# Performance work log

Measured on AMD Instinct MI355X. Metric: run time of the kernel, lower is better.

Reference implementation:

```python
import jax, jax.numpy as jnp
import numpy as np

H = 32  # hidden size


def _lstm_layer(x_sbi, w_ih, w_hh, b_ih, b_hh):
    # x_sbi: [S, B, in]; w_ih: [4H, in]; w_hh: [4H, H] (torch gate order i,f,g,o)
    S, B, _ = x_sbi.shape
    # precompute input projections for all timesteps: [S, B, 4H]
    xg = jnp.einsum('sbi,gi->sbg', x_sbi, w_ih) + (b_ih + b_hh)

    def step(carry, xg_t):
        h, c = carry
        gates = xg_t + h @ w_hh.T  # [B, 4H]
        i, f, g, o = jnp.split(gates, 4, axis=-1)
        i = jax.nn.sigmoid(i)
        f = jax.nn.sigmoid(f)
        g = jnp.tanh(g)
        o = jax.nn.sigmoid(o)
        c = f * c + i * g
        h = o * jnp.tanh(c)
        return (h, c), h

    h0 = jnp.zeros((B, H), x_sbi.dtype)
    c0 = jnp.zeros((B, H), x_sbi.dtype)
    (h_last, _), hs = jax.lax.scan(step, (h0, c0), xg)
    return hs, h_last  # hs: [S, B, H]


def setup_inputs() -> dict:
    key = jax.random.key(0)
    ks = jax.random.split(key, 12)
    B, S = 4096, 512
    s = 1.0 / np.sqrt(H)  # torch default uniform(-1/sqrt(H), 1/sqrt(H))
    u = lambda k, shape: jax.random.uniform(k, shape, jnp.float32, -s, s)
    return {
        'x': jax.random.normal(ks[0], (B, S, 1), jnp.float32),
        'w_ih0': u(ks[1], (4 * H, 1)),
        'w_hh0': u(ks[2], (4 * H, H)),
        'b_ih0': u(ks[3], (4 * H,)),
        'b_hh0': u(ks[4], (4 * H,)),
        'w_ih1': u(ks[5], (4 * H, H)),
        'w_hh1': u(ks[6], (4 * H, H)),
        'b_ih1': u(ks[7], (4 * H,)),
        'b_hh1': u(ks[8], (4 * H,)),
        'fc1_w': u(ks[9], (16, H)),
        'fc1_b': u(ks[9], (16,)),
        'fc2_w': u(ks[10], (1, 16)),
        'fc2_b': u(ks[11], (1,)),
    }


def reference(x, w_ih0, w_hh0, b_ih0, b_hh0, w_ih1, w_hh1, b_ih1, b_hh1,
              fc1_w, fc1_b, fc2_w, fc2_b):
    x_sbi = jnp.swapaxes(x, 0, 1)  # [S, B, 1]
    hs1, _ = _lstm_layer(x_sbi, w_ih0, w_hh0, b_ih0, b_hh0)
    _, h_last = _lstm_layer(hs1, w_ih1, w_hh1, b_ih1, b_hh1)  # last timestep of layer 2
    y = h_last @ fc1_w.T + fc1_b
    y = jnp.where(y >= 0, y, 0.2 * y)  # leaky_relu(0.2)
    y = y @ fc2_w.T + fc2_b
    return y  # [B, 1]
```

## Files before the change

kernel.cpp:

```cpp
#include <hip/hip_runtime.h>

#define H 32
#define SEQ 512
#define BM 16
#define NTHREADS 512
#define HSTRIDE 40

typedef _Float16 half8 __attribute__((ext_vector_type(8)));
typedef __attribute__((ext_vector_type(4))) float f32x4;

#define L2E 1.44269504088896340736f

__device__ __forceinline__ float rcp_(float x)  { return __builtin_amdgcn_rcpf(x); }
__device__ __forceinline__ float exp2_(float x) { return __builtin_amdgcn_exp2f(x); }

__global__ __launch_bounds__(NTHREADS, 2) void lstm_kernel(
    const float* __restrict__ x,
    const float* __restrict__ w_ih0,
    const float* __restrict__ w_hh0,
    const float* __restrict__ b_ih0, const float* __restrict__ b_hh0,
    const float* __restrict__ w_ih1,
    const float* __restrict__ w_hh1,
    const float* __restrict__ b_ih1, const float* __restrict__ b_hh1,
    const float* __restrict__ fc1_w,
    const float* __restrict__ fc1_b,
    const float* __restrict__ fc2_w,
    const float* __restrict__ fc2_b,
    float* __restrict__ out)
{
    __shared__ __align__(16) float    xbufT[SEQ * BM];
    __shared__ __align__(16) _Float16 h1s[2][BM * HSTRIDE];
    __shared__ __align__(16) _Float16 h2s[2][BM * HSTRIDE];
    __shared__ __align__(16) float    h2f[BM * 33];
    __shared__ __align__(16) float    yb[BM * 17];

    const int tid  = threadIdx.x;
    const int lane = tid & 63;
    const int wv   = tid >> 6;
    const int c    = lane & 15;
    const int q    = lane >> 4;
    const int r0   = blockIdx.x * BM;

    {
        const int row = tid >> 5;
        const int s0  = (tid & 31) * 16;
        const float* xr = x + (size_t)(r0 + row) * SEQ + s0;
        #pragma unroll
        for (int i = 0; i < 16; i += 4) {
            float4 v = *(const float4*)&xr[i];
            xbufT[(s0 + i + 0) * BM + row] = v.x;
            xbufT[(s0 + i + 1) * BM + row] = v.y;
            xbufT[(s0 + i + 2) * BM + row] = v.z;
            xbufT[(s0 + i + 3) * BM + row] = v.w;
        }
    }
    for (int i = tid; i < BM * HSTRIDE; i += NTHREADS) {
        h1s[0][i] = (_Float16)0.f; h1s[1][i] = (_Float16)0.f;
        h2s[0][i] = (_Float16)0.f; h2s[1][i] = (_Float16)0.f;
    }

    const float gsc[4] = { -L2E, -L2E, 2.f * L2E, -L2E };
    const int worig = (c & 3) * H + 4 * wv + (c >> 2);
    const float wsc = gsc[c & 3];
    const int kb = 8 * q;
    half8 w0h, w0l, wih, wil, whh, whl;
    {
        const float* p = &w_hh0[worig * H + kb];
        #pragma unroll
        for (int j = 0; j < 8; ++j) { float v = p[j] * wsc; _Float16 h = (_Float16)v; w0h[j] = h; w0l[j] = (_Float16)(v - (float)h); }
        p = &w_ih1[worig * H + kb];
        #pragma unroll
        for (int j = 0; j < 8; ++j) { float v = p[j] * wsc; _Float16 h = (_Float16)v; wih[j] = h; wil[j] = (_Float16)(v - (float)h); }
        p = &w_hh1[worig * H + kb];
        #pragma unroll
        for (int j = 0; j < 8; ++j) { float v = p[j] * wsc; _Float16 h = (_Float16)v; whh[j] = h; whl[j] = (_Float16)(v - (float)h); }
    }

    const int m = c;
    const int u = 4 * wv + q;
    f32x4 bias1v, bias2v;
    float wx[4];
    #pragma unroll
    for (int g = 0; g < 4; ++g) {
        bias1v[g] = (b_ih0[g * H + u] + b_hh0[g * H + u]) * gsc[g];
        bias2v[g] = (b_ih1[g * H + u] + b_hh1[g * H + u]) * gsc[g];
        wx[g]     = w_ih0[g * H + u] * gsc[g];
    }
    float c1 = 0.f, c2 = 0.f, h2last = 0.f;

    const int fofs = c * HSTRIDE + kb;
    const int hofs = m * HSTRIDE + u;

    __syncthreads();

    auto cell = [&](const f32x4& g, float& cst) -> float {
        float ei = exp2_(g[0]);
        float ef = exp2_(g[1]);
        float eg = exp2_(g[2]);
        float eo = exp2_(g[3]);
        float A  = 1.f + ei;
        float F  = 1.f + ef;
        float Gp = eg + 1.f, Gm = eg - 1.f;
        float t1 = A * Gp;
        float num = fmaf(cst, t1, Gm * F);
        float cn  = num * rcp_(F * t1);
        cn = fminf(fmaxf(cn, -12.f), 12.f);
        cst = cn;
        float ec = exp2_(cn * (2.f * L2E));
        return (ec - 1.f) * rcp_((1.f + eo) * (ec + 1.f));
    };

    auto do_step = [&](const _Float16* __restrict__ h1r, const _Float16* __restrict__ h2r,
                       _Float16* __restrict__ h1w, _Float16* __restrict__ h2w,
                       int t, bool ew1, bool ew2) {
        half8 a1 = *(const half8*)(h1r + fofs);
        half8 a2 = *(const half8*)(h2r + fofs);
        float xv = 0.f;
        if (ew1) xv = xbufT[t * BM + m];
        f32x4 g1 = bias1v, g2a = bias2v;
        f32x4 g2b = {0.f, 0.f, 0.f, 0.f};
        g1  = __builtin_amdgcn_mfma_f32_16x16x32_f16(w0h, a1, g1,  0, 0, 0);
        g2a = __builtin_amdgcn_mfma_f32_16x16x32_f16(wih, a1, g2a, 0, 0, 0);
        g2b = __builtin_amdgcn_mfma_f32_16x16x32_f16(whh, a2, g2b, 0, 0, 0);
        g1  = __builtin_amdgcn_mfma_f32_16x16x32_f16(w0l, a1, g1,  0, 0, 0);
        g2a = __builtin_amdgcn_mfma_f32_16x16x32_f16(wil, a1, g2a, 0, 0, 0);
        g2b = __builtin_amdgcn_mfma_f32_16x16x32_f16(whl, a2, g2b, 0, 0, 0);
        if (ew1) {
            #pragma unroll
            for (int j = 0; j < 4; ++j) g1[j] = fmaf(xv, wx[j], g1[j]);
            float h1v = cell(g1, c1);
            h1w[hofs] = (_Float16)h1v;
        }
        if (ew2) {
            f32x4 g2;
            #pragma unroll
            for (int j = 0; j < 4; ++j) g2[j] = g2a[j] + g2b[j];
            float h2v = cell(g2, c2);
            h2last = h2v;
            h2w[hofs] = (_Float16)h2v;
        }
        __syncthreads();
    };

    do_step(h1s[0], h2s[0], h1s[1], h2s[1], 0, true, false);
    for (int tt = 0; tt < 255; ++tt) {
        int t = 1 + 2 * tt;
        do_step(h1s[1], h2s[1], h1s[0], h2s[0], t,     true, true);
        do_step(h1s[0], h2s[0], h1s[1], h2s[1], t + 1, true, true);
    }
    do_step(h1s[1], h2s[1], h1s[0], h2s[0], 511, true, true);
    do_step(h1s[0], h2s[0], h1s[1], h2s[1], 512, false, true);

    h2f[m * 33 + u] = h2last;
    __syncthreads();
    if (tid < BM * 16) {
        int rr = tid >> 4, j = tid & 15;
        float acc = fc1_b[j];
        #pragma unroll
        for (int k = 0; k < H; ++k) acc += fc1_w[j * H + k] * h2f[rr * 33 + k];
        acc = acc >= 0.f ? acc : 0.2f * acc;
        yb[rr * 17 + j] = acc * fc2_w[j];
    }
    __syncthreads();
    if (tid < BM) {
        float acc = fc2_b[0];
        #pragma unroll
        for (int j = 0; j < 16; ++j) acc += yb[tid * 17 + j];
        out[r0 + tid] = acc;
    }
}

extern "C" void kernel_launch(void* const* d_in, const int* in_sizes, int n_in,
                              void* d_out, int out_size, void* d_ws, size_t ws_size,
                              hipStream_t stream) {
    const float* x     = (const float*)d_in[0];
    const float* w_ih0 = (const float*)d_in[1];
    const float* w_hh0 = (const float*)d_in[2];
    const float* b_ih0 = (const float*)d_in[3];
    const float* b_hh0 = (const float*)d_in[4];
    const float* w_ih1 = (const float*)d_in[5];
    const float* w_hh1 = (const float*)d_in[6];
    const float* b_ih1 = (const float*)d_in[7];
    const float* b_hh1 = (const float*)d_in[8];
    const float* fc1_w = (const float*)d_in[9];
    const float* fc1_b = (const float*)d_in[10];
    const float* fc2_w = (const float*)d_in[11];
    const float* fc2_b = (const float*)d_in[12];
    float* out = (float*)d_out;

    const int B = in_sizes[0] / SEQ;
    hipLaunchKernelGGL(lstm_kernel, dim3(B / BM), dim3(NTHREADS), 0, stream,
                       x, w_ih0, w_hh0, b_ih0, b_hh0, w_ih1, w_hh1, b_ih1, b_hh1,
                       fc1_w, fc1_b, fc2_w, fc2_b, out);
}
```

Before: 272.6 us.

## Split LSTM layers across two wave groups with 1024-thread blocks

Doubles the block to 16 waves and gives layer 1 and layer 2 separate wave groups. Each wave now holds weights for only one layer and runs a single cell update per step, where before it ran both. This shortens the per-step critical path and frees registers, at the cost of a larger barrier across 16 waves and possibly fewer resident blocks per CU. The clamp is also changed to a med3 instruction.

```diff
diff --git a/kernel.cpp b/kernel.cpp
--- a/kernel.cpp
+++ b/kernel.cpp
@@ -3,7 +3,7 @@
 #define H 32
 #define SEQ 512
 #define BM 16
-#define NTHREADS 512
+#define NTHREADS 1024
 #define HSTRIDE 40
 
 typedef _Float16 half8 __attribute__((ext_vector_type(8)));
@@ -14,7 +14,7 @@
 __device__ __forceinline__ float rcp_(float x)  { return __builtin_amdgcn_rcpf(x); }
 __device__ __forceinline__ float exp2_(float x) { return __builtin_amdgcn_exp2f(x); }
 
-__global__ __launch_bounds__(NTHREADS, 2) void lstm_kernel(
+__global__ __launch_bounds__(NTHREADS, 4) void lstm_kernel(
     const float* __restrict__ x,
     const float* __restrict__ w_ih0,
     const float* __restrict__ w_hh0,
@@ -37,16 +37,18 @@
     const int tid  = threadIdx.x;
     const int lane = tid & 63;
     const int wv   = tid >> 6;
+    const int grp  = wv >> 3;
+    const int tw   = wv & 7;
     const int c    = lane & 15;
     const int q    = lane >> 4;
     const int r0   = blockIdx.x * BM;
 
     {
-        const int row = tid >> 5;
-        const int s0  = (tid & 31) * 16;
+        const int row = tid >> 6;
+        const int s0  = (tid & 63) * 8;
         const float* xr = x + (size_t)(r0 + row) * SEQ + s0;
         #pragma unroll
-        for (int i = 0; i < 16; i += 4) {
+        for (int i = 0; i < 8; i += 4) {
             float4 v = *(const float4*)&xr[i];
             xbufT[(s0 + i + 0) * BM + row] = v.x;
             xbufT[(s0 + i + 1) * BM + row] = v.y;
@@ -60,40 +62,44 @@
     }
 
     const float gsc[4] = { -L2E, -L2E, 2.f * L2E, -L2E };
-    const int worig = (c & 3) * H + 4 * wv + (c >> 2);
+    const int worig = (c & 3) * H + 4 * tw + (c >> 2);
     const float wsc = gsc[c & 3];
     const int kb = 8 * q;
-    half8 w0h, w0l, wih, wil, whh, whl;
-    {
+    const int m = c;
+    const int u = 4 * tw + q;
+
+    half8 fA, fB, fC, fD;
+    f32x4 biasv;
+    float wx[4] = {0.f, 0.f, 0.f, 0.f};
+    if (grp == 0) {
         const float* p = &w_hh0[worig * H + kb];
         #pragma unroll
-        for (int j = 0; j < 8; ++j) { float v = p[j] * wsc; _Float16 h = (_Float16)v; w0h[j] = h; w0l[j] = (_Float16)(v - (float)h); }
-        p = &w_ih1[worig * H + kb];
-        #pragma unroll
-        for (int j = 0; j < 8; ++j) { float v = p[j] * wsc; _Float16 h = (_Float16)v; wih[j] = h; wil[j] = (_Float16)(v - (float)h); }
+        for (int j = 0; j < 8; ++j) { float v = p[j] * wsc; _Float16 h = (_Float16)v; fA[j] = h; fB[j] = (_Float16)(v - (float)h); }
+        #pragma unroll
+        for (int g = 0; g < 4; ++g) {
+            biasv[g] = (b_ih0[g * H + u] + b_hh0[g * H + u]) * gsc[g];
+            wx[g]    = w_ih0[g * H + u] * gsc[g];
+        }
+    } else {
+        const float* p = &w_ih1[worig * H + kb];
+        #pragma unroll
+        for (int j = 0; j < 8; ++j) { float v = p[j] * wsc; _Float16 h = (_Float16)v; fA[j] = h; fB[j] = (_Float16)(v - (float)h); }
         p = &w_hh1[worig * H + kb];
         #pragma unroll
-        for (int j = 0; j < 8; ++j) { float v = p[j] * wsc; _Float16 h = (_Float16)v; whh[j] = h; whl[j] = (_Float16)(v - (float)h); }
-    }
-
-    const int m = c;
-    const int u = 4 * wv + q;
-    f32x4 bias1v, bias2v;
-    float wx[4];
-    #pragma unroll
-    for (int g = 0; g < 4; ++g) {
-        bias1v[g] = (b_ih0[g * H + u] + b_hh0[g * H + u]) * gsc[g];
-        bias2v[g] = (b_ih1[g * H + u] + b_hh1[g * H + u]) * gsc[g];
-        wx[g]     = w_ih0[g * H + u] * gsc[g];
-    }
-    float c1 = 0.f, c2 = 0.f, h2last = 0.f;
+        for (int j = 0; j < 8; ++j) { float v = p[j] * wsc; _Float16 h = (_Float16)v; fC[j] = h; fD[j] = (_Float16)(v - (float)h); }
+        #pragma unroll
+        for (int g = 0; g < 4; ++g)
+            biasv[g] = (b_ih1[g * H + u] + b_hh1[g * H + u]) * gsc[g];
+    }
+
+    float cst = 0.f, h2last = 0.f;
 
     const int fofs = c * HSTRIDE + kb;
     const int hofs = m * HSTRIDE + u;
 
     __syncthreads();
 
-    auto cell = [&](const f32x4& g, float& cst) -> float {
+    auto cell = [&](const f32x4& g) -> float {
         float ei = exp2_(g[0]);
         float ef = exp2_(g[1]);
         float eg = exp2_(g[2]);
@@ -104,7 +110,7 @@
         float t1 = A * Gp;
         float num = fmaf(cst, t1, Gm * F);
         float cn  = num * rcp_(F * t1);
-        cn = fminf(fmaxf(cn, -12.f), 12.f);
+        cn = __builtin_amdgcn_fmed3f(cn, -12.f, 12.f);
         cst = cn;
         float ec = exp2_(cn * (2.f * L2E));
         return (ec - 1.f) * rcp_((1.f + eo) * (ec + 1.f));
@@ -112,32 +118,36 @@
 
     auto do_step = [&](const _Float16* __restrict__ h1r, const _Float16* __restrict__ h2r,
                        _Float16* __restrict__ h1w, _Float16* __restrict__ h2w,
-                       int t, bool ew1, bool ew2) {
-        half8 a1 = *(const half8*)(h1r + fofs);
-        half8 a2 = *(const half8*)(h2r + fofs);
-        float xv = 0.f;
-        if (ew1) xv = xbufT[t * BM + m];
-        f32x4 g1 = bias1v, g2a = bias2v;
-        f32x4 g2b = {0.f, 0.f, 0.f, 0.f};
-        g1  = __builtin_amdgcn_mfma_f32_16x16x32_f16(w0h, a1, g1,  0, 0, 0);
-        g2a = __builtin_amdgcn_mfma_f32_16x16x32_f16(wih, a1, g2a, 0, 0, 0);
-        g2b = __builtin_amdgcn_mfma_f32_16x16x32_f16(whh, a2, g2b, 0, 0, 0);
-        g1  = __builtin_amdgcn_mfma_f32_16x16x32_f16(w0l, a1, g1,  0, 0, 0);
-        g2a = __builtin_amdgcn_mfma_f32_16x16x32_f16(wil, a1, g2a, 0, 0, 0);
-        g2b = __builtin_amdgcn_mfma_f32_16x16x32_f16(whl, a2, g2b, 0, 0, 0);
-        if (ew1) {
-            #pragma unroll
-            for (int j = 0; j < 4; ++j) g1[j] = fmaf(xv, wx[j], g1[j]);
-            float h1v = cell(g1, c1);
-            h1w[hofs] = (_Float16)h1v;
-        }
-        if (ew2) {
-            f32x4 g2;
-            #pragma unroll
-            for (int j = 0; j < 4; ++j) g2[j] = g2a[j] + g2b[j];
-            float h2v = cell(g2, c2);
-            h2last = h2v;
-            h2w[hofs] = (_Float16)h2v;
+                       int t, bool e1, bool e2) {
+        if (grp == 0) {
+            if (e1) {
+                half8 a1 = *(const half8*)(h1r + fofs);
+                float xv = xbufT[t * BM + m];
+                f32x4 g1 = biasv;
+                g1 = __builtin_amdgcn_mfma_f32_16x16x32_f16(fA, a1, g1, 0, 0, 0);
+                g1 = __builtin_amdgcn_mfma_f32_16x16x32_f16(fB, a1, g1, 0, 0, 0);
+                #pragma unroll
+                for (int j = 0; j < 4; ++j) g1[j] = fmaf(xv, wx[j], g1[j]);
+                float h1v = cell(g1);
+                h1w[hofs] = (_Float16)h1v;
+            }
+        } else {
+            if (e2) {
+                half8 a1 = *(const half8*)(h1r + fofs);
+                half8 a2 = *(const half8*)(h2r + fofs);
+                f32x4 ga = biasv;
+                f32x4 gb = {0.f, 0.f, 0.f, 0.f};
+                ga = __builtin_amdgcn_mfma_f32_16x16x32_f16(fA, a1, ga, 0, 0, 0);
+                gb = __builtin_amdgcn_mfma_f32_16x16x32_f16(fC, a2, gb, 0, 0, 0);
+                ga = __builtin_amdgcn_mfma_f32_16x16x32_f16(fB, a1, ga, 0, 0, 0);
+                gb = __builtin_amdgcn_mfma_f32_16x16x32_f16(fD, a2, gb, 0, 0, 0);
+                f32x4 g2;
+                #pragma unroll
+                for (int j = 0; j < 4; ++j) g2[j] = ga[j] + gb[j];
+                float h2v = cell(g2);
+                h2last = h2v;
+                h2w[hofs] = (_Float16)h2v;
+            }
         }
         __syncthreads();
     };
@@ -151,7 +161,7 @@
     do_step(h1s[1], h2s[1], h1s[0], h2s[0], 511, true, true);
     do_step(h1s[0], h2s[0], h1s[1], h2s[1], 512, false, true);
 
-    h2f[m * 33 + u] = h2last;
+    if (grp == 1) h2f[m * 33 + u] = h2last;
     __syncthreads();
     if (tid < BM * 16) {
         int rr = tid >> 4, j = tid & 15;
```

Result: slower. 291.7 us (+7.0%).

## Halve rows per block and rebalance gate tiles across lanes via bpermute

Applied to the files above, without the earlier changes.

Each block now handles 8 batch rows with 4 waves instead of 16 rows with 8 waves, so the grid doubles. Each wave issues two sets of MFMA gate tiles (A and B hidden-unit halves) whose valid columns are merged with ds_bpermute, so every lane still does exactly one LSTM cell. The intent is a cheaper per-step barrier across fewer waves, and letting two independent blocks interleave on a CU to hide recurrence latency. The cost is twice the MFMA count per wave, with half the MFMA columns wasted on zero rows, plus the cross-lane permute. The clamp is also switched to a med3 instruction.

```diff
diff --git a/kernel.cpp b/kernel.cpp
--- a/kernel.cpp
+++ b/kernel.cpp
@@ -2,8 +2,8 @@
 
 #define H 32
 #define SEQ 512
-#define BM 16
-#define NTHREADS 512
+#define NR 8
+#define NTHREADS 256
 #define HSTRIDE 40
 
 typedef _Float16 half8 __attribute__((ext_vector_type(8)));
@@ -13,6 +13,10 @@
 
 __device__ __forceinline__ float rcp_(float x)  { return __builtin_amdgcn_rcpf(x); }
 __device__ __forceinline__ float exp2_(float x) { return __builtin_amdgcn_exp2f(x); }
+__device__ __forceinline__ float bperm_f(int idx, float v) {
+    return __int_as_float(__builtin_amdgcn_ds_bpermute(idx, __float_as_int(v)));
+}
+#define MFMA16(A, B, C) __builtin_amdgcn_mfma_f32_16x16x32_f16((A), (B), (C), 0, 0, 0)
 
 __global__ __launch_bounds__(NTHREADS, 2) void lstm_kernel(
     const float* __restrict__ x,
@@ -28,18 +32,18 @@
     const float* __restrict__ fc2_b,
     float* __restrict__ out)
 {
-    __shared__ __align__(16) float    xbufT[SEQ * BM];
-    __shared__ __align__(16) _Float16 h1s[2][BM * HSTRIDE];
-    __shared__ __align__(16) _Float16 h2s[2][BM * HSTRIDE];
-    __shared__ __align__(16) float    h2f[BM * 33];
-    __shared__ __align__(16) float    yb[BM * 17];
+    __shared__ __align__(16) float    xbufT[SEQ * NR];
+    __shared__ __align__(16) _Float16 h1s[2][16 * HSTRIDE];
+    __shared__ __align__(16) _Float16 h2s[2][16 * HSTRIDE];
+    __shared__ __align__(16) float    h2f[NR * 33];
+    __shared__ __align__(16) float    yb[NR * 17];
 
     const int tid  = threadIdx.x;
     const int lane = tid & 63;
     const int wv   = tid >> 6;
     const int c    = lane & 15;
     const int q    = lane >> 4;
-    const int r0   = blockIdx.x * BM;
+    const int r0   = blockIdx.x * NR;
 
     {
         const int row = tid >> 5;
@@ -48,48 +52,71 @@
         #pragma unroll
         for (int i = 0; i < 16; i += 4) {
             float4 v = *(const float4*)&xr[i];
-            xbufT[(s0 + i + 0) * BM + row] = v.x;
-            xbufT[(s0 + i + 1) * BM + row] = v.y;
-            xbufT[(s0 + i + 2) * BM + row] = v.z;
-            xbufT[(s0 + i + 3) * BM + row] = v.w;
-        }
-    }
-    for (int i = tid; i < BM * HSTRIDE; i += NTHREADS) {
+            xbufT[(s0 + i + 0) * NR + row] = v.x;
+            xbufT[(s0 + i + 1) * NR + row] = v.y;
+            xbufT[(s0 + i + 2) * NR + row] = v.z;
+            xbufT[(s0 + i + 3) * NR + row] = v.w;
+        }
+    }
+    for (int i = tid; i < 16 * HSTRIDE; i += NTHREADS) {
         h1s[0][i] = (_Float16)0.f; h1s[1][i] = (_Float16)0.f;
         h2s[0][i] = (_Float16)0.f; h2s[1][i] = (_Float16)0.f;
     }
 
     const float gsc[4] = { -L2E, -L2E, 2.f * L2E, -L2E };
-    const int worig = (c & 3) * H + 4 * wv + (c >> 2);
+    const int kb  = 8 * q;
     const float wsc = gsc[c & 3];
-    const int kb = 8 * q;
-    half8 w0h, w0l, wih, wil, whh, whl;
+
+    half8 w0hA, w0lA, w0hB, w0lB;
+    half8 wihA, wilA, wihB, wilB;
+    half8 whhA, whlA, whhB, whlB;
     {
-        const float* p = &w_hh0[worig * H + kb];
-        #pragma unroll
-        for (int j = 0; j < 8; ++j) { float v = p[j] * wsc; _Float16 h = (_Float16)v; w0h[j] = h; w0l[j] = (_Float16)(v - (float)h); }
-        p = &w_ih1[worig * H + kb];
-        #pragma unroll
-        for (int j = 0; j < 8; ++j) { float v = p[j] * wsc; _Float16 h = (_Float16)v; wih[j] = h; wil[j] = (_Float16)(v - (float)h); }
-        p = &w_hh1[worig * H + kb];
-        #pragma unroll
-        for (int j = 0; j < 8; ++j) { float v = p[j] * wsc; _Float16 h = (_Float16)v; whh[j] = h; whl[j] = (_Float16)(v - (float)h); }
-    }
-
-    const int m = c;
-    const int u = 4 * wv + q;
-    f32x4 bias1v, bias2v;
+        const int wrA = (c & 3) * H + 4 * wv + (c >> 2);
+        const int wrB = (c & 3) * H + 4 * (wv + 4) + (c >> 2);
+        const float *pA, *pB;
+        pA = &w_hh0[wrA * H + kb]; pB = &w_hh0[wrB * H + kb];
+        #pragma unroll
+        for (int j = 0; j < 8; ++j) {
+            float vA = pA[j] * wsc; _Float16 hA = (_Float16)vA; w0hA[j] = hA; w0lA[j] = (_Float16)(vA - (float)hA);
+            float vB = pB[j] * wsc; _Float16 hB = (_Float16)vB; w0hB[j] = hB; w0lB[j] = (_Float16)(vB - (float)hB);
+        }
+        pA = &w_ih1[wrA * H + kb]; pB = &w_ih1[wrB * H + kb];
+        #pragma unroll
+        for (int j = 0; j < 8; ++j) {
+            float vA = pA[j] * wsc; _Float16 hA = (_Float16)vA; wihA[j] = hA; wilA[j] = (_Float16)(vA - (float)hA);
+            float vB = pB[j] * wsc; _Float16 hB = (_Float16)vB; wihB[j] = hB; wilB[j] = (_Float16)(vB - (float)hB);
+        }
+        pA = &w_hh1[wrA * H + kb]; pB = &w_hh1[wrB * H + kb];
+        #pragma unroll
+        for (int j = 0; j < 8; ++j) {
+            float vA = pA[j] * wsc; _Float16 hA = (_Float16)vA; whhA[j] = hA; whlA[j] = (_Float16)(vA - (float)hA);
+            float vB = pB[j] * wsc; _Float16 hB = (_Float16)vB; whhB[j] = hB; whlB[j] = (_Float16)(vB - (float)hB);
+        }
+    }
+
+    f32x4 b1A, b1B, b2A, b2B;
+    {
+        const int uA = 4 * wv + q, uB = 4 * (wv + 4) + q;
+        #pragma unroll
+        for (int j = 0; j < 4; ++j) {
+            b1A[j] = (b_ih0[j * H + uA] + b_hh0[j * H + uA]) * gsc[j];
+            b1B[j] = (b_ih0[j * H + uB] + b_hh0[j * H + uB]) * gsc[j];
+            b2A[j] = (b_ih1[j * H + uA] + b_hh1[j * H + uA]) * gsc[j];
+            b2B[j] = (b_ih1[j * H + uB] + b_hh1[j * H + uB]) * gsc[j];
+        }
+    }
+
+    const int prow  = lane & 7;
+    const int upost = 4 * (wv + 4 * ((lane >> 3) & 1)) + (lane >> 4);
     float wx[4];
     #pragma unroll
-    for (int g = 0; g < 4; ++g) {
-        bias1v[g] = (b_ih0[g * H + u] + b_hh0[g * H + u]) * gsc[g];
-        bias2v[g] = (b_ih1[g * H + u] + b_hh1[g * H + u]) * gsc[g];
-        wx[g]     = w_ih0[g * H + u] * gsc[g];
-    }
+    for (int j = 0; j < 4; ++j) wx[j] = w_ih0[j * H + upost] * gsc[j];
+
     float c1 = 0.f, c2 = 0.f, h2last = 0.f;
 
-    const int fofs = c * HSTRIDE + kb;
-    const int hofs = m * HSTRIDE + u;
+    const int fofs  = c * HSTRIDE + kb;
+    const int whofs = prow * HSTRIDE + upost;
+    const int bpi   = (lane & ~8) * 4;
 
     __syncthreads();
 
@@ -104,40 +131,52 @@
         float t1 = A * Gp;
         float num = fmaf(cst, t1, Gm * F);
         float cn  = num * rcp_(F * t1);
-        cn = fminf(fmaxf(cn, -12.f), 12.f);
+        cn = __builtin_amdgcn_fmed3f(cn, -12.f, 12.f);
         cst = cn;
         float ec = exp2_(cn * (2.f * L2E));
         return (ec - 1.f) * rcp_((1.f + eo) * (ec + 1.f));
     };
 
+    const bool takeB = (lane & 8) != 0;
+    auto rebal = [&](const f32x4& A, const f32x4& B) -> f32x4 {
+        f32x4 r;
+        #pragma unroll
+        for (int j = 0; j < 4; ++j) {
+            float pb = bperm_f(bpi, B[j]);
+            r[j] = takeB ? pb : A[j];
+        }
+        return r;
+    };
+
     auto do_step = [&](const _Float16* __restrict__ h1r, const _Float16* __restrict__ h2r,
                        _Float16* __restrict__ h1w, _Float16* __restrict__ h2w,
-                       int t, bool ew1, bool ew2) {
+                       int t, bool e1, bool e2) {
         half8 a1 = *(const half8*)(h1r + fofs);
         half8 a2 = *(const half8*)(h2r + fofs);
-        float xv = 0.f;
-        if (ew1) xv = xbufT[t * BM + m];
-        f32x4 g1 = bias1v, g2a = bias2v;
-        f32x4 g2b = {0.f, 0.f, 0.f, 0.f};
-        g1  = __builtin_amdgcn_mfma_f32_16x16x32_f16(w0h, a1, g1,  0, 0, 0);
-        g2a = __builtin_amdgcn_mfma_f32_16x16x32_f16(wih, a1, g2a, 0, 0, 0);
-        g2b = __builtin_amdgcn_mfma_f32_16x16x32_f16(whh, a2, g2b, 0, 0, 0);
-        g1  = __builtin_amdgcn_mfma_f32_16x16x32_f16(w0l, a1, g1,  0, 0, 0);
-        g2a = __builtin_amdgcn_mfma_f32_16x16x32_f16(wil, a1, g2a, 0, 0, 0);
-        g2b = __builtin_amdgcn_mfma_f32_16x16x32_f16(whl, a2, g2b, 0, 0, 0);
-        if (ew1) {
+        f32x4 g1A = b1A, g1B = b1B, gaA = b2A, gaB = b2B;
+        f32x4 gbA = {0.f, 0.f, 0.f, 0.f}, gbB = {0.f, 0.f, 0.f, 0.f};
+        g1A = MFMA16(w0hA, a1, g1A);  g1B = MFMA16(w0hB, a1, g1B);
+        gaA = MFMA16(wihA, a1, gaA);  gaB = MFMA16(wihB, a1, gaB);
+        gbA = MFMA16(whhA, a2, gbA);  gbB = MFMA16(whhB, a2, gbB);
+        g1A = MFMA16(w0lA, a1, g1A);  g1B = MFMA16(w0lB, a1, g1B);
+        gaA = MFMA16(wilA, a1, gaA);  gaB = MFMA16(wilB, a1, gaB);
+        gbA = MFMA16(whlA, a2, gbA);  gbB = MFMA16(whlB, a2, gbB);
+        f32x4 g2A, g2B;
+        #pragma unroll
+        for (int j = 0; j < 4; ++j) { g2A[j] = gaA[j] + gbA[j]; g2B[j] = gaB[j] + gbB[j]; }
+        f32x4 g1 = rebal(g1A, g1B);
+        f32x4 g2 = rebal(g2A, g2B);
+        if (e1) {
+            float xv = xbufT[t * NR + prow];
             #pragma unroll
             for (int j = 0; j < 4; ++j) g1[j] = fmaf(xv, wx[j], g1[j]);
             float h1v = cell(g1, c1);
-            h1w[hofs] = (_Float16)h1v;
-        }
-        if (ew2) {
-            f32x4 g2;
-            #pragma unroll
-            for (int j = 0; j < 4; ++j) g2[j] = g2a[j] + g2b[j];
+            h1w[whofs] = (_Float16)h1v;
+        }
+        if (e2) {
             float h2v = cell(g2, c2);
             h2last = h2v;
-            h2w[hofs] = (_Float16)h2v;
+            h2w[whofs] = (_Float16)h2v;
         }
         __syncthreads();
     };
@@ -151,9 +190,9 @@
     do_step(h1s[1], h2s[1], h1s[0], h2s[0], 511, true, true);
     do_step(h1s[0], h2s[0], h1s[1], h2s[1], 512, false, true);
 
-    h2f[m * 33 + u] = h2last;
+    h2f[prow * 33 + upost] = h2last;
     __syncthreads();
-    if (tid < BM * 16) {
+    if (tid < NR * 16) {
         int rr = tid >> 4, j = tid & 15;
         float acc = fc1_b[j];
         #pragma unroll
@@ -162,7 +201,7 @@
         yb[rr * 17 + j] = acc * fc2_w[j];
     }
     __syncthreads();
-    if (tid < BM) {
+    if (tid < NR) {
         float acc = fc2_b[0];
         #pragma unroll
         for (int j = 0; j < 16; ++j) acc += yb[tid * 17 + j];
@@ -189,7 +228,7 @@
     float* out = (float*)d_out;
 
     const int B = in_sizes[0] / SEQ;
-    hipLaunchKernelGGL(lstm_kernel, dim3(B / BM), dim3(NTHREADS), 0, stream,
+    hipLaunchKernelGGL(lstm_kernel, dim3(B / NR), dim3(NTHREADS), 0, stream,
                        x, w_ih0, w_hh0, b_ih0, b_hh0, w_ih1, w_hh1, b_ih1, b_hh1,
                        fc1_w, fc1_b, fc2_w, fc2_b, out);
 }
```

Result: slower. 365.2 us (+34.0%).

## Swizzle LDS hidden-state layout, share reciprocals across layers, chain MFMAs

Applied to the files above, without the earlier changes.

Applies an XOR swizzle to the fp16 hidden-state LDS reads and writes to cut bank conflicts. When both layers are active, the two LSTM cells are merged so each pair of divisions uses a single reciprocal, trading extra multiplies for fewer rcp instructions. Layer-2 MFMAs are chained into one accumulator instead of two summed ones, and clamping uses fmed3. Sharing one reciprocal between both cells slightly changes rounding and could overflow when the products of denominators grow large.

```diff
diff --git a/kernel.cpp b/kernel.cpp
--- a/kernel.cpp
+++ b/kernel.cpp
@@ -13,6 +13,7 @@
 
 __device__ __forceinline__ float rcp_(float x)  { return __builtin_amdgcn_rcpf(x); }
 __device__ __forceinline__ float exp2_(float x) { return __builtin_amdgcn_exp2f(x); }
+#define MFMA16(A, B, C) __builtin_amdgcn_mfma_f32_16x16x32_f16((A), (B), (C), 0, 0, 0)
 
 __global__ __launch_bounds__(NTHREADS, 2) void lstm_kernel(
     const float* __restrict__ x,
@@ -88,56 +89,70 @@
     }
     float c1 = 0.f, c2 = 0.f, h2last = 0.f;
 
-    const int fofs = c * HSTRIDE + kb;
-    const int hofs = m * HSTRIDE + u;
+    const int fofs  = c * HSTRIDE + ((q ^ (c >> 3)) << 3);
+    const int whofs = m * HSTRIDE + (((u >> 3) ^ (m >> 3)) << 3) + (u & 7);
 
     __syncthreads();
 
-    auto cell = [&](const f32x4& g, float& cst) -> float {
-        float ei = exp2_(g[0]);
-        float ef = exp2_(g[1]);
-        float eg = exp2_(g[2]);
-        float eo = exp2_(g[3]);
-        float A  = 1.f + ei;
-        float F  = 1.f + ef;
+    auto cell1 = [&](const f32x4& g, float& cst) -> float {
+        float ei = exp2_(g[0]), ef = exp2_(g[1]), eg = exp2_(g[2]), eo = exp2_(g[3]);
+        float A = 1.f + ei, F = 1.f + ef;
         float Gp = eg + 1.f, Gm = eg - 1.f;
         float t1 = A * Gp;
         float num = fmaf(cst, t1, Gm * F);
-        float cn  = num * rcp_(F * t1);
-        cn = fminf(fmaxf(cn, -12.f), 12.f);
+        float cn  = __builtin_amdgcn_fmed3f(num * rcp_(F * t1), -12.f, 12.f);
         cst = cn;
         float ec = exp2_(cn * (2.f * L2E));
         return (ec - 1.f) * rcp_((1.f + eo) * (ec + 1.f));
     };
 
+    auto cell2 = [&](const f32x4& ga, const f32x4& gb, float& ha, float& hb) {
+        float eia = exp2_(ga[0]), efa = exp2_(ga[1]), ega = exp2_(ga[2]), eoa = exp2_(ga[3]);
+        float eib = exp2_(gb[0]), efb = exp2_(gb[1]), egb = exp2_(gb[2]), eob = exp2_(gb[3]);
+        float Aa = 1.f + eia, Fa = 1.f + efa, Gpa = ega + 1.f, Gma = ega - 1.f;
+        float Ab = 1.f + eib, Fb = 1.f + efb, Gpb = egb + 1.f, Gmb = egb - 1.f;
+        float t1a = Aa * Gpa,  t1b = Ab * Gpb;
+        float Da  = Fa * t1a,  Db  = Fb * t1b;
+        float r   = rcp_(Da * Db);
+        float na  = fmaf(c1, t1a, Gma * Fa);
+        float nb  = fmaf(c2, t1b, Gmb * Fb);
+        c1 = __builtin_amdgcn_fmed3f(na * (r * Db), -12.f, 12.f);
+        c2 = __builtin_amdgcn_fmed3f(nb * (r * Da), -12.f, 12.f);
+        float eca = exp2_(c1 * (2.f * L2E));
+        float ecb = exp2_(c2 * (2.f * L2E));
+        float Ea  = (1.f + eoa) * (eca + 1.f);
+        float Eb  = (1.f + eob) * (ecb + 1.f);
+        float r2  = rcp_(Ea * Eb);
+        ha = (eca - 1.f) * (r2 * Eb);
+        hb = (ecb - 1.f) * (r2 * Ea);
+    };
+
     auto do_step = [&](const _Float16* __restrict__ h1r, const _Float16* __restrict__ h2r,
                        _Float16* __restrict__ h1w, _Float16* __restrict__ h2w,
-                       int t, bool ew1, bool ew2) {
+                       int t, bool e1, bool e2) {
         half8 a1 = *(const half8*)(h1r + fofs);
         half8 a2 = *(const half8*)(h2r + fofs);
         float xv = 0.f;
-        if (ew1) xv = xbufT[t * BM + m];
-        f32x4 g1 = bias1v, g2a = bias2v;
-        f32x4 g2b = {0.f, 0.f, 0.f, 0.f};
-        g1  = __builtin_amdgcn_mfma_f32_16x16x32_f16(w0h, a1, g1,  0, 0, 0);
-        g2a = __builtin_amdgcn_mfma_f32_16x16x32_f16(wih, a1, g2a, 0, 0, 0);
-        g2b = __builtin_amdgcn_mfma_f32_16x16x32_f16(whh, a2, g2b, 0, 0, 0);
-        g1  = __builtin_amdgcn_mfma_f32_16x16x32_f16(w0l, a1, g1,  0, 0, 0);
-        g2a = __builtin_amdgcn_mfma_f32_16x16x32_f16(wil, a1, g2a, 0, 0, 0);
-        g2b = __builtin_amdgcn_mfma_f32_16x16x32_f16(whl, a2, g2b, 0, 0, 0);
-        if (ew1) {
+        if (e1) xv = xbufT[t * BM + m];
+        f32x4 g1 = MFMA16(w0l, a1, MFMA16(w0h, a1, bias1v));
+        f32x4 g2 = MFMA16(whl, a2, MFMA16(whh, a2, MFMA16(wil, a1, MFMA16(wih, a1, bias2v))));
+        if (e1) {
             #pragma unroll
             for (int j = 0; j < 4; ++j) g1[j] = fmaf(xv, wx[j], g1[j]);
-            float h1v = cell(g1, c1);
-            h1w[hofs] = (_Float16)h1v;
         }
-        if (ew2) {
-            f32x4 g2;
-            #pragma unroll
-            for (int j = 0; j < 4; ++j) g2[j] = g2a[j] + g2b[j];
-            float h2v = cell(g2, c2);
+        if (e1 && e2) {
+            float h1v, h2v;
+            cell2(g1, g2, h1v, h2v);
             h2last = h2v;
-            h2w[hofs] = (_Float16)h2v;
+            h1w[whofs] = (_Float16)h1v;
+            h2w[whofs] = (_Float16)h2v;
+        } else if (e1) {
+            float h1v = cell1(g1, c1);
+            h1w[whofs] = (_Float16)h1v;
+        } else if (e2) {
+            float h2v = cell1(g2, c2);
+            h2last = h2v;
+            h2w[whofs] = (_Float16)h2v;
         }
         __syncthreads();
     };
```

Result: slower. 279.6 us (+2.5%).
